# Optimization experiments

Measured on AMD Instinct MI355X. Metric: run time of the kernel, lower is better.

Reference implementation:

```python
import jax, jax.numpy as jnp
import numpy as np

B, NM, NA, D = 16, 4000, 128, 128  # scenes, map nodes/scene, agents/scene, feature dim
DIST_TH = 7.0
BOX = 100.0


def _gn(x, g, b, eps=1e-5):
    # GroupNorm with 1 group over [N, C]: per-row normalization, biased variance, affine.
    mu = jnp.mean(x, axis=-1, keepdims=True)
    var = jnp.mean((x - mu) ** 2, axis=-1, keepdims=True)
    return (x - mu) * jax.lax.rsqrt(var + eps) * g + b


def _forward(feat, turn, control, intersect, agents, map_ctrs, agent_ctrs,
             meta_w, meta_g, meta_b,
             dist_w1, dist_b1, dist_w2, dist_g2, dist_b2,
             query_w, query_g, query_b,
             ctx_w1, ctx_g1, ctx_b1, ctx_w2,
             agt_w, norm_g, norm_b,
             lin_w, lin_g, lin_b,
             hi, wi):
    relu = jax.nn.relu
    # meta fuse: cat(feat, turn, control, intersect) -> Linear(n_map+4 -> n_map) + GN + ReLU
    x = jnp.concatenate([feat, turn, control[:, None], intersect[:, None]], axis=1)
    x = relu(_gn(x @ meta_w.T, meta_g, meta_b))
    for i in range(2):  # two Att layers with distinct weights
        res = x
        d = map_ctrs[hi] - agent_ctrs[wi]                         # [E, 2]
        d = relu(d @ dist_w1[i].T + dist_b1[i])                   # [E, D]
        d = relu(_gn(d @ dist_w2[i].T, dist_g2[i], dist_b2[i]))
        q = relu(_gn(x[hi] @ query_w[i].T, query_g[i], query_b[i]))
        c = jnp.concatenate([d, q, agents[wi]], axis=1)           # [E, 3D]
        c = relu(_gn(c @ ctx_w1[i].T, ctx_g1[i], ctx_b1[i]))
        c = c @ ctx_w2[i].T                                       # [E, D]
        x = x @ agt_w[i].T                                        # [N, D]
        x = x.at[hi].add(c)                                       # index_add_ scatter
        x = relu(_gn(x, norm_g[i], norm_b[i]))
        x = _gn(x @ lin_w[i].T, lin_g[i], lin_b[i])               # Linear act=False
        x = relu(x + res)
    return x


def setup_inputs() -> dict:
    # edge list (hi: map node, wi: agent) built exactly like Att's per-scene dist<=th nonzero
    rng = np.random.default_rng(0)
    mc = rng.uniform(0.0, BOX, (B, NM, 2)).astype(np.float32)
    ac = rng.uniform(0.0, BOX, (B, NA, 2)).astype(np.float32)
    dist = np.sqrt(((mc[:, :, None, :] - ac[:, None, :, :]) ** 2).sum(-1))
    bb, h, w = np.nonzero(dist <= DIST_TH)
    hi = jnp.asarray((bb * NM + h).astype(np.int32))
    wi = jnp.asarray((bb * NA + w).astype(np.int32))

    key = jax.random.key(0)
    ks = jax.random.split(key, 20)
    s = 0.02
    nrm = lambda k, shape: jax.random.normal(k, shape, jnp.float32) * s
    return {
        "feat": jax.random.normal(ks[0], (B * NM, D), jnp.float32),
        "turn": jax.random.normal(ks[1], (B * NM, 2), jnp.float32),
        "control": jax.random.uniform(ks[2], (B * NM,), jnp.float32),
        "intersect": jax.random.uniform(ks[3], (B * NM,), jnp.float32),
        "agents": jax.random.normal(ks[4], (B * NA, D), jnp.float32),
        "map_ctrs": jnp.asarray(mc.reshape(-1, 2)),
        "agent_ctrs": jnp.asarray(ac.reshape(-1, 2)),
        "meta_w": nrm(ks[5], (D, D + 4)),
        "meta_g": jnp.ones((D,), jnp.float32),
        "meta_b": jnp.zeros((D,), jnp.float32),
        "dist_w1": nrm(ks[6], (2, D, 2)),
        "dist_b1": nrm(ks[7], (2, D)),
        "dist_w2": nrm(ks[8], (2, D, D)),
        "dist_g2": jnp.ones((2, D), jnp.float32),
        "dist_b2": jnp.zeros((2, D), jnp.float32),
        "query_w": nrm(ks[9], (2, D, D)),
        "query_g": jnp.ones((2, D), jnp.float32),
        "query_b": jnp.zeros((2, D), jnp.float32),
        "ctx_w1": nrm(ks[10], (2, D, 3 * D)),
        "ctx_g1": jnp.ones((2, D), jnp.float32),
        "ctx_b1": jnp.zeros((2, D), jnp.float32),
        "ctx_w2": nrm(ks[11], (2, D, D)),
        "agt_w": nrm(ks[12], (2, D, D)),
        "norm_g": jnp.ones((2, D), jnp.float32),
        "norm_b": jnp.zeros((2, D), jnp.float32),
        "lin_w": nrm(ks[13], (2, D, D)),
        "lin_g": jnp.ones((2, D), jnp.float32),
        "lin_b": jnp.zeros((2, D), jnp.float32),
        "hi": hi,
        "wi": wi,
    }


def reference(feat, turn, control, intersect, agents, map_ctrs, agent_ctrs,
              meta_w, meta_g, meta_b,
              dist_w1, dist_b1, dist_w2, dist_g2, dist_b2,
              query_w, query_g, query_b,
              ctx_w1, ctx_g1, ctx_b1, ctx_w2,
              agt_w, norm_g, norm_b,
              lin_w, lin_g, lin_b,
              hi, wi):
    return _forward(feat, turn, control, intersect, agents, map_ctrs, agent_ctrs,
                    meta_w, meta_g, meta_b,
                    dist_w1, dist_b1, dist_w2, dist_g2, dist_b2,
                    query_w, query_g, query_b,
                    ctx_w1, ctx_g1, ctx_b1, ctx_w2,
                    agt_w, norm_g, norm_b,
                    lin_w, lin_g, lin_b,
                    hi, wi)
```

## Files before the change

kernel.cpp:

```cpp
#include <hip/hip_runtime.h>


typedef __attribute__((ext_vector_type(8))) short short8v;
typedef __attribute__((ext_vector_type(4))) float f32x4;

#define NXCD 8

__device__ __forceinline__ unsigned short f2b(float f) {
    union { float f; unsigned u; } v; v.f = f;
    return (unsigned short)((v.u + 0x7fffu + ((v.u >> 16) & 1u)) >> 16);
}
__device__ __forceinline__ unsigned pk2(float a, float b) {
    return (unsigned)f2b(a) | ((unsigned)f2b(b) << 16);
}
__device__ __forceinline__ float bflo(unsigned u) { return __uint_as_float(u << 16); }
__device__ __forceinline__ float bfhi(unsigned u) { return __uint_as_float(u & 0xffff0000u); }

union U4S8 { unsigned u[4]; short8v v; };

__device__ __forceinline__ void bar_lds() {
    __builtin_amdgcn_sched_barrier(0);
    asm volatile("s_waitcnt lgkmcnt(0)" ::: "memory");
    __builtin_amdgcn_s_barrier();
    __builtin_amdgcn_sched_barrier(0);
}

template<int NV>
__device__ __forceinline__ void sload(short8v (&v)[NV], const unsigned short* __restrict__ src,
                                      int t) {
#pragma unroll
    for (int i = 0; i < NV; i++) v[i] = *(const short8v*)(src + (size_t)i * 2048 + t * 8);
}
template<int NV>
__device__ __forceinline__ void swrite(unsigned short* dst, const short8v (&v)[NV], int t) {
#pragma unroll
    for (int i = 0; i < NV; i++) *(short8v*)(dst + i * 2048 + t * 8) = v[i];
}

template<int NK>
__device__ __forceinline__ void wgemm_lds(const unsigned short* Wlds,
                                          const short8v* bf, f32x4 (&acc)[8], int l) {
#pragma unroll
    for (int mt = 0; mt < 8; mt++) {
        acc[mt] = (f32x4){0.f, 0.f, 0.f, 0.f};
#pragma unroll
        for (int kk = 0; kk < NK; kk++) {
            const short8v a = *(const short8v*)(Wlds + ((mt * NK + kk) * 64 + l) * 8);
            acc[mt] = __builtin_amdgcn_mfma_f32_16x16x32_bf16(a, bf[kk], acc[mt], 0, 0, 0);
        }
    }
}

__device__ __forceinline__ void gn_apply8(f32x4 (&acc)[8], const float* __restrict__ g,
                                          const float* __restrict__ b, int lg, bool relu) {
    float s = 0.f, s2 = 0.f;
#pragma unroll
    for (int mt = 0; mt < 8; mt++)
#pragma unroll
        for (int q = 0; q < 4; q++) { const float v = acc[mt][q]; s += v; s2 += v * v; }
    s += __shfl_xor(s, 16, 64); s2 += __shfl_xor(s2, 16, 64);
    s += __shfl_xor(s, 32, 64); s2 += __shfl_xor(s2, 32, 64);
    const float mu = s * (1.f / 128.f);
    const float rs = rsqrtf(s2 * (1.f / 128.f) - mu * mu + 1e-5f);
#pragma unroll
    for (int mt = 0; mt < 8; mt++) {
        const f32x4 g4 = *(const f32x4*)(g + mt * 16 + lg * 4);
        const f32x4 b4 = *(const f32x4*)(b + mt * 16 + lg * 4);
#pragma unroll
        for (int q = 0; q < 4; q++) {
            float y = (acc[mt][q] - mu) * rs * g4[q] + b4[q];
            acc[mt][q] = relu ? fmaxf(y, 0.f) : y;
        }
    }
}

__device__ __forceinline__ void pack_p(const f32x4 (&acc)[8], unsigned (&p)[8][2]) {
#pragma unroll
    for (int mt = 0; mt < 8; mt++) {
        p[mt][0] = pk2(acc[mt][0], acc[mt][1]);
        p[mt][1] = pk2(acc[mt][2], acc[mt][3]);
    }
}

__device__ __forceinline__ void lds_put(unsigned short* wbuf, const unsigned (&p)[8][2],
                                        int lg, int col) {
#pragma unroll
    for (int mt = 0; mt < 8; mt++) {
        const unsigned long long v = (unsigned long long)p[mt][0] |
                                     ((unsigned long long)p[mt][1] << 32);
        *(unsigned long long*)((char*)wbuf + ((col * 256 + mt * 32 + lg * 8) ^ ((col & 7) << 4))) = v;
    }
}
__device__ __forceinline__ void lds_wait() {
    asm volatile("s_waitcnt lgkmcnt(0)" ::: "memory");
    __builtin_amdgcn_sched_barrier(0);
}
__device__ __forceinline__ void lds_get(const unsigned short* wbuf, int lg, int col,
                                        short8v* bf) {
#pragma unroll
    for (int kk = 0; kk < 4; kk++)
        bf[kk] = *(const short8v*)((const char*)wbuf +
                 ((col * 256 + kk * 64 + lg * 16) ^ ((col & 7) << 4)));
}
__device__ __forceinline__ void relayout1(unsigned short* wbuf, int lg, int col,
                                          f32x4 (&acc)[8], short8v* bf) {
    unsigned p[8][2];
    pack_p(acc, p); lds_put(wbuf, p, lg, col); lds_wait(); lds_get(wbuf, lg, col, bf);
}

__device__ __forceinline__ void load_bfrag_row(const float* __restrict__ src, int lg,
                                               short8v* bf) {
#pragma unroll
    for (int kk = 0; kk < 4; kk++) {
        const f32x4 a = *(const f32x4*)(src + kk * 32 + lg * 8);
        const f32x4 b = *(const f32x4*)(src + kk * 32 + lg * 8 + 4);
        U4S8 u;
        u.u[0] = pk2(a[0], a[1]); u.u[1] = pk2(a[2], a[3]);
        u.u[2] = pk2(b[0], b[1]); u.u[3] = pk2(b[2], b[3]);
        bf[kk] = u.v;
    }
}
__device__ __forceinline__ void store_rows(float* dst, const f32x4 (&acc)[8], int lg) {
#pragma unroll
    for (int mt = 0; mt < 8; mt++) *(f32x4*)(dst + mt * 16 + lg * 4) = acc[mt];
}
__device__ __forceinline__ void store_rows_bf16(unsigned short* dst, const f32x4 (&acc)[8], int lg) {
#pragma unroll
    for (int mt = 0; mt < 8; mt++) {
        uint2 u; u.x = pk2(acc[mt][0], acc[mt][1]); u.y = pk2(acc[mt][2], acc[mt][3]);
        *(uint2*)(dst + mt * 16 + lg * 4) = u;
    }
}
__device__ __forceinline__ void residual_add_bf16(f32x4 (&acc)[8],
                                                  const unsigned short* __restrict__ rp,
                                                  int lg, bool relu) {
#pragma unroll
    for (int mt = 0; mt < 8; mt++) {
        const uint2 u = *(const uint2*)(rp + mt * 16 + lg * 4);
        acc[mt][0] += bflo(u.x); acc[mt][1] += bfhi(u.x);
        acc[mt][2] += bflo(u.y); acc[mt][3] += bfhi(u.y);
        if (relu) {
#pragma unroll
            for (int q = 0; q < 4; q++) acc[mt][q] = fmaxf(acc[mt][q], 0.f);
        }
    }
}
__device__ __forceinline__ void gather_issue(const unsigned short* __restrict__ Qc,
                                             const unsigned short* __restrict__ Acp,
                                             int h, int w, int lg,
                                             uint2 (&qv)[8], uint2 (&av)[8]) {
    const int hl = (h < 0) ? 0 : h;
    const unsigned short* qp = Qc  + (size_t)hl * 128 + lg * 4;
    const unsigned short* ap = Acp + (size_t)w  * 128 + lg * 4;
#pragma unroll
    for (int mt = 0; mt < 8; mt++) {
        qv[mt] = *(const uint2*)(qp + mt * 16);
        av[mt] = *(const uint2*)(ap + mt * 16);
    }
}
__device__ __forceinline__ void gather_add(f32x4 (&acc)[8], const uint2 (&qv)[8],
                                           const uint2 (&av)[8]) {
#pragma unroll
    for (int mt = 0; mt < 8; mt++) {
        acc[mt][0] += bflo(qv[mt].x) + bflo(av[mt].x);
        acc[mt][1] += bfhi(qv[mt].x) + bfhi(av[mt].x);
        acc[mt][2] += bflo(qv[mt].y) + bflo(av[mt].y);
        acc[mt][3] += bfhi(qv[mt].y) + bfhi(av[mt].y);
    }
}
__device__ __forceinline__ void build_d1(const float* __restrict__ dw1,
                                         const float* __restrict__ db1,
                                         float dx, float dy, int lg, short8v* bf) {
#pragma unroll
    for (int kk = 0; kk < 4; kk++) {
        U4S8 u;
#pragma unroll
        for (int ii = 0; ii < 4; ii++) {
            const int c0 = kk * 32 + lg * 8 + ii * 2;
            const float2 wa = *(const float2*)(dw1 + 2 * c0);
            const float2 wb = *(const float2*)(dw1 + 2 * c0 + 2);
            const float2 bb = *(const float2*)(db1 + c0);
            u.u[ii] = pk2(fmaxf(fmaf(wa.x, dx, fmaf(wa.y, dy, bb.x)), 0.f),
                          fmaxf(fmaf(wb.x, dx, fmaf(wb.y, dy, bb.y)), 0.f));
        }
        bf[kk] = u.v;
    }
}

struct PrepJob { const float* src; int dst; int ld; int kmax; int nk; };
struct PrepJobs { PrepJob j[17]; };

__global__ __launch_bounds__(64) void prep_weights(PrepJobs P, unsigned short* __restrict__ pool) {
    const PrepJob J = P.j[blockIdx.y];
    const int f = blockIdx.x;
    if (f >= 8 * J.nk) return;
    const int l = threadIdx.x;
    const int n = (f / J.nk) * 16 + (l & 15);
    const int kb = (f % J.nk) * 32 + (l >> 4) * 8;
    float v[8];
#pragma unroll
    for (int i = 0; i < 8; i++) {
        const int k = kb + i;
        v[i] = (k < J.kmax) ? J.src[(size_t)n * J.ld + k] : 0.f;
    }
    U4S8 u;
#pragma unroll
    for (int i = 0; i < 4; i++) u.u[i] = pk2(v[2 * i], v[2 * i + 1]);
    *(short8v*)(pool + J.dst + ((size_t)f * 64 + l) * 8) = u.v;
}

__device__ __forceinline__ void agent_path(
    unsigned short* Wlds, int abid, int NA, const float* __restrict__ agents,
    const unsigned short* __restrict__ Wc1a, unsigned short* Ac,
    int t, int wid, int l, int lg, int col)
{
    short8v sv[8];
    sload<8>(sv, Wc1a, t);
    const int r = abid * 64 + wid * 16 + col;
    const int rc = min(r, NA - 1);
    short8v bf[4];
    load_bfrag_row(agents + (size_t)rc * 128, lg, bf);
    swrite<8>(Wlds, sv, t);
    bar_lds();
    f32x4 acc[8];
    wgemm_lds<4>(Wlds, bf, acc, l);
    if (r < NA) store_rows_bf16(Ac + (size_t)r * 128, acc, lg);
}

__global__ __launch_bounds__(256, 2) void meta_node(
    const int N, const int NA, const int gN,
    const float* __restrict__ feat, const float* __restrict__ turn,
    const float* __restrict__ ctrl, const float* __restrict__ inter,
    const float* __restrict__ agents,
    const unsigned short* __restrict__ Wm,
    const float* __restrict__ mg, const float* __restrict__ mb,
    const unsigned short* __restrict__ Wagt, const unsigned short* __restrict__ Wq,
    const float* __restrict__ qg, const float* __restrict__ qb,
    const unsigned short* __restrict__ Wc1q, const unsigned short* __restrict__ Wc1a,
    unsigned short* __restrict__ xA, float* __restrict__ xB,
    unsigned short* __restrict__ Qc, unsigned short* __restrict__ Ac)
{
    __shared__ unsigned short Wlds[20480];
    __shared__ unsigned short wbuf[4][2048];
    const int t = threadIdx.x, wid = t >> 6, l = t & 63, lg = l >> 4, col = l & 15;
    if (blockIdx.x >= gN) {
        agent_path(Wlds, blockIdx.x - gN, NA, agents, Wc1a, Ac, t, wid, l, lg, col);
        return;
    }
    const int r = blockIdx.x * 64 + wid * 16 + col;
    const int rc = min(r, N - 1);

    short8v s10[10];
    sload<10>(s10, Wm, t);
    short8v bf[5];
    load_bfrag_row(feat + (size_t)rc * 128, lg, bf);
    {
        U4S8 u; u.u[0] = 0; u.u[1] = 0; u.u[2] = 0; u.u[3] = 0;
        if (lg == 0) {
            const float2 tv = *(const float2*)(turn + (size_t)rc * 2);
            u.u[0] = pk2(tv.x, tv.y);
            u.u[1] = pk2(ctrl[rc], inter[rc]);
        }
        bf[4] = u.v;
    }
    swrite<10>(Wlds, s10, t);
    bar_lds();

    short8v s8[8];
    sload<8>(s8, Wagt, t);
    f32x4 acc[8];
    wgemm_lds<5>(Wlds, bf, acc, l);
    gn_apply8(acc, mg, mb, lg, true);
    if (r < N) store_rows_bf16(xA + (size_t)r * 128, acc, lg);
    short8v bx[4];
    relayout1(wbuf[wid], lg, col, acc, bx);
    bar_lds();
    swrite<8>(Wlds, s8, t);
    bar_lds();

    sload<8>(s8, Wq, t);
    wgemm_lds<4>(Wlds, bx, acc, l);
    if (r < N) store_rows(xB + (size_t)r * 128, acc, lg);
    bar_lds();
    swrite<8>(Wlds, s8, t);
    bar_lds();

    sload<8>(s8, Wc1q, t);
    wgemm_lds<4>(Wlds, bx, acc, l);
    gn_apply8(acc, qg, qb, lg, true);
    relayout1(wbuf[wid], lg, col, acc, bx);
    bar_lds();
    swrite<8>(Wlds, s8, t);
    bar_lds();

    wgemm_lds<4>(Wlds, bx, acc, l);
    if (r < N) store_rows_bf16(Qc + (size_t)r * 128, acc, lg);
}

__device__ __forceinline__ void post_load_gn(const float* xp,
                                             const float* __restrict__ ng,
                                             const float* __restrict__ nb,
                                             int lg, short8v* bf) {
    float v[4][8];
    float s = 0.f, s2 = 0.f;
#pragma unroll
    for (int kk = 0; kk < 4; kk++) {
        *(f32x4*)(v[kk])     = *(const f32x4*)(xp + kk * 32 + lg * 8);
        *(f32x4*)(v[kk] + 4) = *(const f32x4*)(xp + kk * 32 + lg * 8 + 4);
#pragma unroll
        for (int i = 0; i < 8; i++) { s += v[kk][i]; s2 += v[kk][i] * v[kk][i]; }
    }
    s += __shfl_xor(s, 16, 64); s2 += __shfl_xor(s2, 16, 64);
    s += __shfl_xor(s, 32, 64); s2 += __shfl_xor(s2, 32, 64);
    const float mu = s * (1.f / 128.f);
    const float rs = rsqrtf(s2 * (1.f / 128.f) - mu * mu + 1e-5f);
#pragma unroll
    for (int kk = 0; kk < 4; kk++) {
        float y[8];
#pragma unroll
        for (int i = 0; i < 8; i += 4) {
            const f32x4 g4 = *(const f32x4*)(ng + kk * 32 + lg * 8 + i);
            const f32x4 b4 = *(const f32x4*)(nb + kk * 32 + lg * 8 + i);
#pragma unroll
            for (int q = 0; q < 4; q++)
                y[i + q] = fmaxf((v[kk][i + q] - mu) * rs * g4[q] + b4[q], 0.f);
        }
        U4S8 u;
#pragma unroll
        for (int i = 0; i < 4; i++) u.u[i] = pk2(y[2 * i], y[2 * i + 1]);
        bf[kk] = u.v;
    }
}

__global__ __launch_bounds__(256, 3) void post_node(
    const int N, const int NA, const int gN,
    const float* __restrict__ ng, const float* __restrict__ nb,
    const unsigned short* __restrict__ Wlin,
    const float* __restrict__ lgam, const float* __restrict__ lbet,
    const float* __restrict__ agents, const unsigned short* __restrict__ Wc1a,
    const unsigned short* __restrict__ Wagt, const unsigned short* __restrict__ Wq,
    const float* __restrict__ qg, const float* __restrict__ qb,
    const unsigned short* __restrict__ Wc1q,
    unsigned short* xA, float* xB,
    unsigned short* __restrict__ Qc, unsigned short* __restrict__ Ac)
{
    __shared__ unsigned short Wlds[16384];
    __shared__ unsigned short wbuf[4][2048];
    const int t = threadIdx.x, wid = t >> 6, l = t & 63, lg = l >> 4, col = l & 15;
    if (blockIdx.x >= gN) {
        agent_path(Wlds, blockIdx.x - gN, NA, agents, Wc1a, Ac, t, wid, l, lg, col);
        return;
    }
    const int r = blockIdx.x * 64 + wid * 16 + col;
    const int rc = min(r, N - 1);

    short8v s8[8];
    sload<8>(s8, Wlin, t);
    short8v bf[4];
    post_load_gn(xB + (size_t)rc * 128, ng, nb, lg, bf);
    swrite<8>(Wlds, s8, t);
    bar_lds();

    sload<8>(s8, Wagt, t);
    f32x4 acc[8];
    wgemm_lds<4>(Wlds, bf, acc, l);
    gn_apply8(acc, lgam, lbet, lg, false);
    residual_add_bf16(acc, xA + (size_t)rc * 128, lg, true);
    if (r < N) store_rows_bf16(xA + (size_t)r * 128, acc, lg);
    short8v bx[4];
    relayout1(wbuf[wid], lg, col, acc, bx);
    bar_lds();
    swrite<8>(Wlds, s8, t);
    bar_lds();

    sload<8>(s8, Wq, t);
    wgemm_lds<4>(Wlds, bx, acc, l);
    if (r < N) store_rows(xB + (size_t)r * 128, acc, lg);
    bar_lds();
    swrite<8>(Wlds, s8, t);
    bar_lds();

    sload<8>(s8, Wc1q, t);
    wgemm_lds<4>(Wlds, bx, acc, l);
    gn_apply8(acc, qg, qb, lg, true);
    relayout1(wbuf[wid], lg, col, acc, bx);
    bar_lds();
    swrite<8>(Wlds, s8, t);
    bar_lds();

    wgemm_lds<4>(Wlds, bx, acc, l);
    if (r < N) store_rows_bf16(Qc + (size_t)r * 128, acc, lg);
}

__global__ __launch_bounds__(256, 4) void post_final(
    const int N,
    const float* __restrict__ xB,
    const float* __restrict__ ng, const float* __restrict__ nb,
    const unsigned short* __restrict__ Wlin,
    const float* __restrict__ lgam, const float* __restrict__ lbet,
    const unsigned short* __restrict__ res, float* __restrict__ out)
{
    __shared__ unsigned short Wlds[16384];
    const int t = threadIdx.x, wid = t >> 6, l = t & 63, lg = l >> 4, col = l & 15;
    const int r = blockIdx.x * 64 + wid * 16 + col;
    const int rc = min(r, N - 1);
    short8v s8[8];
    sload<8>(s8, Wlin, t);
    short8v bf[4];
    post_load_gn(xB + (size_t)rc * 128, ng, nb, lg, bf);
    swrite<8>(Wlds, s8, t);
    bar_lds();
    f32x4 acc[8];
    wgemm_lds<4>(Wlds, bf, acc, l);
    gn_apply8(acc, lgam, lbet, lg, false);
    residual_add_bf16(acc, res + (size_t)rc * 128, lg, true);
    if (r < N) store_rows(out + (size_t)r * 128, acc, lg);
}

__global__ __launch_bounds__(256, 3) void edge_mfma(
    const int E, const int nwg,
    const int* __restrict__ hi, const int* __restrict__ wi,
    const float* __restrict__ mc, const float* __restrict__ ac,
    const float* __restrict__ dw1, const float* __restrict__ db1,
    const unsigned short* __restrict__ Wd2, const float* __restrict__ dg2, const float* __restrict__ db2,
    const unsigned short* __restrict__ Wc1d, const float* __restrict__ cg1, const float* __restrict__ cb1,
    const unsigned short* __restrict__ Wc2,
    const unsigned short* __restrict__ Qc, const unsigned short* __restrict__ Acp,
    float* __restrict__ OUT)
{
    __shared__ unsigned short Wlds[16384];
    __shared__ unsigned short wbuf[4][2048];
    __shared__ int s_h[64];
    const int t = threadIdx.x, wid = t >> 6, l = t & 63, lg = l >> 4, col = l & 15;

    int bid;
    {
        const int orig = blockIdx.x;
        const int q = nwg / NXCD, r = nwg % NXCD;
        const int xcd = orig % NXCD, i = orig / NXCD;
        bid = (xcd < r ? xcd * (q + 1) : r * (q + 1) + (xcd - r) * q) + i;
    }
    const int eidx = bid * 64 + wid * 16 + col;

    short8v s8[8];
    sload<8>(s8, Wd2, t);

    int h = -1, w = 0;
    if (eidx < E) { h = hi[eidx]; w = wi[eidx]; }
    if (lg == 0) s_h[wid * 16 + col] = h;
    const int hl = (h < 0) ? 0 : h;
    const float2 mcv = *(const float2*)(mc + 2 * (size_t)hl);
    const float2 acv = *(const float2*)(ac + 2 * (size_t)w);
    const float dx = mcv.x - acv.x, dy = mcv.y - acv.y;

    uint2 qv[8], av[8];
    gather_issue(Qc, Acp, h, w, lg, qv, av);

    short8v bf[4];
    build_d1(dw1, db1, dx, dy, lg, bf);

    swrite<8>(Wlds, s8, t);
    bar_lds();

    sload<8>(s8, Wc1d, t);
    f32x4 acc[8];
    wgemm_lds<4>(Wlds, bf, acc, l);
    gn_apply8(acc, dg2, db2, lg, true);
    relayout1(wbuf[wid], lg, col, acc, bf);
    bar_lds();
    swrite<8>(Wlds, s8, t);
    bar_lds();

    sload<8>(s8, Wc2, t);
    wgemm_lds<4>(Wlds, bf, acc, l);
    gather_add(acc, qv, av);
    gn_apply8(acc, cg1, cb1, lg, true);
    relayout1(wbuf[wid], lg, col, acc, bf);
    bar_lds();
    swrite<8>(Wlds, s8, t);
    bar_lds();

    wgemm_lds<4>(Wlds, bf, acc, l);
    unsigned p[8][2];
    pack_p(acc, p); lds_put(wbuf[wid], p, lg, col); lds_wait();

#pragma unroll
    for (int pass = 0; pass < 2; pass++) {
        const int c = pass * 64 + l;
        float pend = 0.f; int ph = -1;
#pragma unroll
        for (int e = 0; e < 16; e++) {
            const int he = s_h[wid * 16 + e];
            const unsigned short uv = *(const unsigned short*)((const char*)wbuf[wid] +
                                      ((e * 256 + c * 2) ^ ((e & 7) << 4)));
            const float v = __uint_as_float((unsigned)uv << 16);
            if (he == ph) pend += v;
            else {
                if (ph >= 0) atomicAdd(&OUT[(size_t)ph * 128 + c], pend);
                ph = he; pend = v;
            }
        }
        if (ph >= 0) atomicAdd(&OUT[(size_t)ph * 128 + c], pend);
    }
}

extern "C" void kernel_launch(void* const* d_in, const int* in_sizes, int n_in,
                              void* d_out, int out_size, void* d_ws, size_t ws_size,
                              hipStream_t stream)
{
    const float* feat    = (const float*)d_in[0];
    const float* turn    = (const float*)d_in[1];
    const float* ctrl    = (const float*)d_in[2];
    const float* inter   = (const float*)d_in[3];
    const float* agents  = (const float*)d_in[4];
    const float* mc      = (const float*)d_in[5];
    const float* ac      = (const float*)d_in[6];
    const float* meta_w  = (const float*)d_in[7];
    const float* meta_g  = (const float*)d_in[8];
    const float* meta_b  = (const float*)d_in[9];
    const float* dist_w1 = (const float*)d_in[10];
    const float* dist_b1 = (const float*)d_in[11];
    const float* dist_w2 = (const float*)d_in[12];
    const float* dist_g2 = (const float*)d_in[13];
    const float* dist_b2 = (const float*)d_in[14];
    const float* query_w = (const float*)d_in[15];
    const float* query_g = (const float*)d_in[16];
    const float* query_b = (const float*)d_in[17];
    const float* ctx_w1  = (const float*)d_in[18];
    const float* ctx_g1  = (const float*)d_in[19];
    const float* ctx_b1  = (const float*)d_in[20];
    const float* ctx_w2  = (const float*)d_in[21];
    const float* agt_w   = (const float*)d_in[22];
    const float* norm_g  = (const float*)d_in[23];
    const float* norm_b  = (const float*)d_in[24];
    const float* lin_w   = (const float*)d_in[25];
    const float* lin_g   = (const float*)d_in[26];
    const float* lin_b   = (const float*)d_in[27];
    const int*   hi      = (const int*)d_in[28];
    const int*   wi      = (const int*)d_in[29];

    const int E  = in_sizes[28];
    const int N  = in_sizes[0] / 128;
    const int NA = in_sizes[4] / 128;

    unsigned short* xA = (unsigned short*)d_ws;
    float* xB = (float*)(xA + (size_t)N * 128);
    unsigned short* pool = (unsigned short*)(xB + (size_t)N * 128);

    const int FR128  = 8 * 4 * 64 * 8;
    const int FRMETA = 8 * 5 * 64 * 8;
    const int POOL_ELEMS = FRMETA + 16 * FR128;

    unsigned short* Ac = pool + POOL_ELEMS;
    unsigned short* Qc = (unsigned short*)d_out;

    PrepJobs P;
    P.j[0] = { meta_w, 0, 132, 132, 5 };
    for (int i = 0; i < 2; i++) {
        const int b = FRMETA + i * 8 * FR128;
        P.j[1 + i * 8 + 0] = { query_w + (size_t)i * 16384, b + 0 * FR128, 128, 128, 4 };
        P.j[1 + i * 8 + 1] = { agt_w   + (size_t)i * 16384, b + 1 * FR128, 128, 128, 4 };
        P.j[1 + i * 8 + 2] = { dist_w2 + (size_t)i * 16384, b + 2 * FR128, 128, 128, 4 };
        P.j[1 + i * 8 + 3] = { ctx_w1  + (size_t)i * 49152,       b + 3 * FR128, 384, 128, 4 };
        P.j[1 + i * 8 + 4] = { ctx_w1  + (size_t)i * 49152 + 128, b + 4 * FR128, 384, 128, 4 };
        P.j[1 + i * 8 + 5] = { ctx_w2  + (size_t)i * 16384, b + 5 * FR128, 128, 128, 4 };
        P.j[1 + i * 8 + 6] = { lin_w   + (size_t)i * 16384, b + 6 * FR128, 128, 128, 4 };
        P.j[1 + i * 8 + 7] = { ctx_w1  + (size_t)i * 49152 + 256, b + 7 * FR128, 384, 128, 4 };
    }
    prep_weights<<<dim3(40, 17), 64, 0, stream>>>(P, pool);

    const int gN = (N + 63) / 64;
    const int gA = (NA + 63) / 64;
    const int gE = (E + 63) / 64;

    const unsigned short* W0 = pool + FRMETA;
    const unsigned short* W1 = pool + FRMETA + 8 * FR128;

    meta_node<<<gN + gA, 256, 0, stream>>>(
        N, NA, gN, feat, turn, ctrl, inter, agents,
        pool, meta_g, meta_b,
        W0 + 1 * FR128, W0 + 0 * FR128, query_g, query_b,
        W0 + 4 * FR128, W0 + 7 * FR128,
        xA, xB, Qc, Ac);

    edge_mfma<<<gE, 256, 0, stream>>>(
        E, gE, hi, wi, mc, ac,
        dist_w1, dist_b1,
        W0 + 2 * FR128, dist_g2, dist_b2,
        W0 + 3 * FR128, ctx_g1, ctx_b1,
        W0 + 5 * FR128, Qc, Ac, xB);

    post_node<<<gN + gA, 256, 0, stream>>>(
        N, NA, gN,
        norm_g, norm_b, W0 + 6 * FR128, lin_g, lin_b,
        agents, W1 + 7 * FR128,
        W1 + 1 * FR128, W1 + 0 * FR128, query_g + 128, query_b + 128,
        W1 + 4 * FR128,
        xA, xB, Qc, Ac);

    edge_mfma<<<gE, 256, 0, stream>>>(
        E, gE, hi, wi, mc, ac,
        dist_w1 + 256, dist_b1 + 128,
        W1 + 2 * FR128, dist_g2 + 128, dist_b2 + 128,
        W1 + 3 * FR128, ctx_g1 + 128, ctx_b1 + 128,
        W1 + 5 * FR128, Qc, Ac, xB);

    post_final<<<gN, 256, 0, stream>>>(
        N, xB, norm_g + 128, norm_b + 128,
        W1 + 6 * FR128, lin_g + 128, lin_b + 128, xA, (float*)d_out);
}
```

Measured before the change: 202.7 us.

## Process 64 rows per wave to amortize LDS weight staging across four subtiles

Each wave now handles four 16-row subtiles (256 rows per block) in all node, agent, final and edge kernels, so every LDS weight load and barrier is reused across four MFMA passes instead of one. The intent is to cut the per-row cost of staging weight fragments and synchronising, and the grid shrinks by four. The edge kernel also double-buffers the Qc/Ac gathers across subtiles and carries the segmented atomic accumulation across subtiles so runs of equal destination rows merge. Register pressure rises sharply (bf arrays of 4x4 or 4x5), launch bounds drop to 2 blocks per CU, and the smaller grid may underfill the GPU.

After: 259.8 us. 1.28x slower.

```diff
diff --git a/kernel.cpp b/kernel.cpp
--- a/kernel.cpp
+++ b/kernel.cpp
@@ -216,15 +216,20 @@
 {
     short8v sv[8];
     sload<8>(sv, Wc1a, t);
-    const int r = abid * 64 + wid * 16 + col;
-    const int rc = min(r, NA - 1);
-    short8v bf[4];
-    load_bfrag_row(agents + (size_t)rc * 128, lg, bf);
+    const int rbase = abid * 256 + wid * 64;
+    short8v bf[4][4];
+#pragma unroll
+    for (int s = 0; s < 4; s++)
+        load_bfrag_row(agents + (size_t)min(rbase + s * 16 + col, NA - 1) * 128, lg, bf[s]);
     swrite<8>(Wlds, sv, t);
     bar_lds();
     f32x4 acc[8];
-    wgemm_lds<4>(Wlds, bf, acc, l);
-    if (r < NA) store_rows_bf16(Ac + (size_t)r * 128, acc, lg);
+#pragma unroll
+    for (int s = 0; s < 4; s++) {
+        const int r = rbase + s * 16 + col;
+        wgemm_lds<4>(Wlds, bf[s], acc, l);
+        if (r < NA) store_rows_bf16(Ac + (size_t)r * 128, acc, lg);
+    }
 }
 
 __global__ __launch_bounds__(256, 2) void meta_node(
@@ -247,21 +252,22 @@
         agent_path(Wlds, blockIdx.x - gN, NA, agents, Wc1a, Ac, t, wid, l, lg, col);
         return;
     }
-    const int r = blockIdx.x * 64 + wid * 16 + col;
-    const int rc = min(r, N - 1);
+    const int rbase = blockIdx.x * 256 + wid * 64;
 
     short8v s10[10];
     sload<10>(s10, Wm, t);
-    short8v bf[5];
-    load_bfrag_row(feat + (size_t)rc * 128, lg, bf);
-    {
+    short8v bf[4][5];
+#pragma unroll
+    for (int s = 0; s < 4; s++) {
+        const int rc = min(rbase + s * 16 + col, N - 1);
+        load_bfrag_row(feat + (size_t)rc * 128, lg, bf[s]);
         U4S8 u; u.u[0] = 0; u.u[1] = 0; u.u[2] = 0; u.u[3] = 0;
         if (lg == 0) {
             const float2 tv = *(const float2*)(turn + (size_t)rc * 2);
             u.u[0] = pk2(tv.x, tv.y);
             u.u[1] = pk2(ctrl[rc], inter[rc]);
         }
-        bf[4] = u.v;
+        bf[s][4] = u.v;
     }
     swrite<10>(Wlds, s10, t);
     bar_lds();
@@ -269,32 +275,46 @@
     short8v s8[8];
     sload<8>(s8, Wagt, t);
     f32x4 acc[8];
-    wgemm_lds<5>(Wlds, bf, acc, l);
-    gn_apply8(acc, mg, mb, lg, true);
-    if (r < N) store_rows_bf16(xA + (size_t)r * 128, acc, lg);
-    short8v bx[4];
-    relayout1(wbuf[wid], lg, col, acc, bx);
+#pragma unroll
+    for (int s = 0; s < 4; s++) {
+        const int r = rbase + s * 16 + col;
+        wgemm_lds<5>(Wlds, bf[s], acc, l);
+        gn_apply8(acc, mg, mb, lg, true);
+        if (r < N) store_rows_bf16(xA + (size_t)r * 128, acc, lg);
+        relayout1(wbuf[wid], lg, col, acc, bf[s]);
+    }
     bar_lds();
     swrite<8>(Wlds, s8, t);
     bar_lds();
 
     sload<8>(s8, Wq, t);
-    wgemm_lds<4>(Wlds, bx, acc, l);
-    if (r < N) store_rows(xB + (size_t)r * 128, acc, lg);
+#pragma unroll
+    for (int s = 0; s < 4; s++) {
+        const int r = rbase + s * 16 + col;
+        wgemm_lds<4>(Wlds, bf[s], acc, l);
+        if (r < N) store_rows(xB + (size_t)r * 128, acc, lg);
+    }
     bar_lds();
     swrite<8>(Wlds, s8, t);
     bar_lds();
 
     sload<8>(s8, Wc1q, t);
-    wgemm_lds<4>(Wlds, bx, acc, l);
-    gn_apply8(acc, qg, qb, lg, true);
-    relayout1(wbuf[wid], lg, col, acc, bx);
-    bar_lds();
-    swrite<8>(Wlds, s8, t);
-    bar_lds();
-
-    wgemm_lds<4>(Wlds, bx, acc, l);
-    if (r < N) store_rows_bf16(Qc + (size_t)r * 128, acc, lg);
+#pragma unroll
+    for (int s = 0; s < 4; s++) {
+        wgemm_lds<4>(Wlds, bf[s], acc, l);
+        gn_apply8(acc, qg, qb, lg, true);
+        relayout1(wbuf[wid], lg, col, acc, bf[s]);
+    }
+    bar_lds();
+    swrite<8>(Wlds, s8, t);
+    bar_lds();
+
+#pragma unroll
+    for (int s = 0; s < 4; s++) {
+        const int r = rbase + s * 16 + col;
+        wgemm_lds<4>(Wlds, bf[s], acc, l);
+        if (r < N) store_rows_bf16(Qc + (size_t)r * 128, acc, lg);
+    }
 }
 
 __device__ __forceinline__ void post_load_gn(const float* xp,
@@ -332,7 +352,7 @@
     }
 }
 
-__global__ __launch_bounds__(256, 3) void post_node(
+__global__ __launch_bounds__(256, 2) void post_node(
     const int N, const int NA, const int gN,
     const float* __restrict__ ng, const float* __restrict__ nb,
     const unsigned short* __restrict__ Wlin,
@@ -351,48 +371,64 @@
         agent_path(Wlds, blockIdx.x - gN, NA, agents, Wc1a, Ac, t, wid, l, lg, col);
         return;
     }
-    const int r = blockIdx.x * 64 + wid * 16 + col;
-    const int rc = min(r, N - 1);
+    const int rbase = blockIdx.x * 256 + wid * 64;
 
     short8v s8[8];
     sload<8>(s8, Wlin, t);
-    short8v bf[4];
-    post_load_gn(xB + (size_t)rc * 128, ng, nb, lg, bf);
+    short8v bf[4][4];
+#pragma unroll
+    for (int s = 0; s < 4; s++)
+        post_load_gn(xB + (size_t)min(rbase + s * 16 + col, N - 1) * 128, ng, nb, lg, bf[s]);
     swrite<8>(Wlds, s8, t);
     bar_lds();
 
     sload<8>(s8, Wagt, t);
     f32x4 acc[8];
-    wgemm_lds<4>(Wlds, bf, acc, l);
-    gn_apply8(acc, lgam, lbet, lg, false);
-    residual_add_bf16(acc, xA + (size_t)rc * 128, lg, true);
-    if (r < N) store_rows_bf16(xA + (size_t)r * 128, acc, lg);
-    short8v bx[4];
-    relayout1(wbuf[wid], lg, col, acc, bx);
+#pragma unroll
+    for (int s = 0; s < 4; s++) {
+        const int r = rbase + s * 16 + col;
+        const int rc = min(r, N - 1);
+        wgemm_lds<4>(Wlds, bf[s], acc, l);
+        gn_apply8(acc, lgam, lbet, lg, false);
+        residual_add_bf16(acc, xA + (size_t)rc * 128, lg, true);
+        if (r < N) store_rows_bf16(xA + (size_t)r * 128, acc, lg);
+        relayout1(wbuf[wid], lg, col, acc, bf[s]);
+    }
     bar_lds();
     swrite<8>(Wlds, s8, t);
     bar_lds();
 
     sload<8>(s8, Wq, t);
-    wgemm_lds<4>(Wlds, bx, acc, l);
-    if (r < N) store_rows(xB + (size_t)r * 128, acc, lg);
+#pragma unroll
+    for (int s = 0; s < 4; s++) {
+        const int r = rbase + s * 16 + col;
+        wgemm_lds<4>(Wlds, bf[s], acc, l);
+        if (r < N) store_rows(xB + (size_t)r * 128, acc, lg);
+    }
     bar_lds();
     swrite<8>(Wlds, s8, t);
     bar_lds();
 
     sload<8>(s8, Wc1q, t);
-    wgemm_lds<4>(Wlds, bx, acc, l);
-    gn_apply8(acc, qg, qb, lg, true);
-    relayout1(wbuf[wid], lg, col, acc, bx);
-    bar_lds();
-    swrite<8>(Wlds, s8, t);
-    bar_lds();
-
-    wgemm_lds<4>(Wlds, bx, acc, l);
-    if (r < N) store_rows_bf16(Qc + (size_t)r * 128, acc, lg);
-}
-
-__global__ __launch_bounds__(256, 4) void post_final(
+#pragma unroll
+    for (int s = 0; s < 4; s++) {
+        wgemm_lds<4>(Wlds, bf[s], acc, l);
+        gn_apply8(acc, qg, qb, lg, true);
+        relayout1(wbuf[wid], lg, col, acc, bf[s]);
+    }
+    bar_lds();
+    swrite<8>(Wlds, s8, t);
+    bar_lds();
+
+#pragma unroll
+    for (int s = 0; s < 4; s++) {
+        const int r = rbase + s * 16 + col;
+        wgemm_lds<4>(Wlds, bf[s], acc, l);
+        if (r < N) store_rows_bf16(Qc + (size_t)r * 128, acc, lg);
+    }
+}
+
+__global__ __launch_bounds__(256, 2) void post_final(
     const int N,
     const float* __restrict__ xB,
     const float* __restrict__ ng, const float* __restrict__ nb,
@@ -402,22 +438,28 @@
 {
     __shared__ unsigned short Wlds[16384];
     const int t = threadIdx.x, wid = t >> 6, l = t & 63, lg = l >> 4, col = l & 15;
-    const int r = blockIdx.x * 64 + wid * 16 + col;
-    const int rc = min(r, N - 1);
+    const int rbase = blockIdx.x * 256 + wid * 64;
     short8v s8[8];
     sload<8>(s8, Wlin, t);
-    short8v bf[4];
-    post_load_gn(xB + (size_t)rc * 128, ng, nb, lg, bf);
+    short8v bf[4][4];
+#pragma unroll
+    for (int s = 0; s < 4; s++)
+        post_load_gn(xB + (size_t)min(rbase + s * 16 + col, N - 1) * 128, ng, nb, lg, bf[s]);
     swrite<8>(Wlds, s8, t);
     bar_lds();
     f32x4 acc[8];
-    wgemm_lds<4>(Wlds, bf, acc, l);
-    gn_apply8(acc, lgam, lbet, lg, false);
-    residual_add_bf16(acc, res + (size_t)rc * 128, lg, true);
-    if (r < N) store_rows(out + (size_t)r * 128, acc, lg);
-}
-
-__global__ __launch_bounds__(256, 3) void edge_mfma(
+#pragma unroll
+    for (int s = 0; s < 4; s++) {
+        const int r = rbase + s * 16 + col;
+        const int rc = min(r, N - 1);
+        wgemm_lds<4>(Wlds, bf[s], acc, l);
+        gn_apply8(acc, lgam, lbet, lg, false);
+        residual_add_bf16(acc, res + (size_t)rc * 128, lg, true);
+        if (r < N) store_rows(out + (size_t)r * 128, acc, lg);
+    }
+}
+
+__global__ __launch_bounds__(256, 2) void edge_mfma(
     const int E, const int nwg,
     const int* __restrict__ hi, const int* __restrict__ wi,
     const float* __restrict__ mc, const float* __restrict__ ac,
@@ -430,7 +472,7 @@
 {
     __shared__ unsigned short Wlds[16384];
     __shared__ unsigned short wbuf[4][2048];
-    __shared__ int s_h[64];
+    __shared__ int s_h[256];
     const int t = threadIdx.x, wid = t >> 6, l = t & 63, lg = l >> 4, col = l & 15;
 
     int bid;
@@ -440,67 +482,87 @@
         const int xcd = orig % NXCD, i = orig / NXCD;
         bid = (xcd < r ? xcd * (q + 1) : r * (q + 1) + (xcd - r) * q) + i;
     }
-    const int eidx = bid * 64 + wid * 16 + col;
+    const int ebase = bid * 256 + wid * 64;
 
     short8v s8[8];
     sload<8>(s8, Wd2, t);
 
-    int h = -1, w = 0;
-    if (eidx < E) { h = hi[eidx]; w = wi[eidx]; }
-    if (lg == 0) s_h[wid * 16 + col] = h;
-    const int hl = (h < 0) ? 0 : h;
-    const float2 mcv = *(const float2*)(mc + 2 * (size_t)hl);
-    const float2 acv = *(const float2*)(ac + 2 * (size_t)w);
-    const float dx = mcv.x - acv.x, dy = mcv.y - acv.y;
-
-    uint2 qv[8], av[8];
-    gather_issue(Qc, Acp, h, w, lg, qv, av);
-
-    short8v bf[4];
-    build_d1(dw1, db1, dx, dy, lg, bf);
+    int h4[4], w4[4];
+    float dx4[4], dy4[4];
+#pragma unroll
+    for (int s = 0; s < 4; s++) {
+        const int eidx = ebase + s * 16 + col;
+        int h = -1, w = 0;
+        if (eidx < E) { h = hi[eidx]; w = wi[eidx]; }
+        h4[s] = h; w4[s] = w;
+        if (lg == 0) s_h[wid * 64 + s * 16 + col] = h;
+        const int hl = (h < 0) ? 0 : h;
+        const float2 mcv = *(const float2*)(mc + 2 * (size_t)hl);
+        const float2 acv = *(const float2*)(ac + 2 * (size_t)w);
+        dx4[s] = mcv.x - acv.x; dy4[s] = mcv.y - acv.y;
+    }
 
     swrite<8>(Wlds, s8, t);
     bar_lds();
 
     sload<8>(s8, Wc1d, t);
+    short8v bf2[4][4];
     f32x4 acc[8];
-    wgemm_lds<4>(Wlds, bf, acc, l);
-    gn_apply8(acc, dg2, db2, lg, true);
-    relayout1(wbuf[wid], lg, col, acc, bf);
+#pragma unroll
+    for (int s = 0; s < 4; s++) {
+        short8v bft[4];
+        build_d1(dw1, db1, dx4[s], dy4[s], lg, bft);
+        wgemm_lds<4>(Wlds, bft, acc, l);
+        gn_apply8(acc, dg2, db2, lg, true);
+        relayout1(wbuf[wid], lg, col, acc, bf2[s]);
+    }
     bar_lds();
     swrite<8>(Wlds, s8, t);
     bar_lds();
 
     sload<8>(s8, Wc2, t);
-    wgemm_lds<4>(Wlds, bf, acc, l);
-    gather_add(acc, qv, av);
-    gn_apply8(acc, cg1, cb1, lg, true);
-    relayout1(wbuf[wid], lg, col, acc, bf);
-    bar_lds();
-    swrite<8>(Wlds, s8, t);
-    bar_lds();
-
-    wgemm_lds<4>(Wlds, bf, acc, l);
-    unsigned p[8][2];
-    pack_p(acc, p); lds_put(wbuf[wid], p, lg, col); lds_wait();
-
-#pragma unroll
-    for (int pass = 0; pass < 2; pass++) {
-        const int c = pass * 64 + l;
-        float pend = 0.f; int ph = -1;
+    uint2 qv[2][8], av[2][8];
+    gather_issue(Qc, Acp, h4[0], w4[0], lg, qv[0], av[0]);
+#pragma unroll
+    for (int s = 0; s < 4; s++) {
+        if (s < 3) gather_issue(Qc, Acp, h4[s + 1], w4[s + 1], lg, qv[(s + 1) & 1], av[(s + 1) & 1]);
+        wgemm_lds<4>(Wlds, bf2[s], acc, l);
+        gather_add(acc, qv[s & 1], av[s & 1]);
+        gn_apply8(acc, cg1, cb1, lg, true);
+        relayout1(wbuf[wid], lg, col, acc, bf2[s]);
+    }
+    bar_lds();
+    swrite<8>(Wlds, s8, t);
+    bar_lds();
+
+    float p0 = 0.f, p1 = 0.f; int ph = -1;
+#pragma unroll
+    for (int s = 0; s < 4; s++) {
+        wgemm_lds<4>(Wlds, bf2[s], acc, l);
+        unsigned p[8][2];
+        pack_p(acc, p); lds_put(wbuf[wid], p, lg, col); lds_wait();
 #pragma unroll
         for (int e = 0; e < 16; e++) {
-            const int he = s_h[wid * 16 + e];
-            const unsigned short uv = *(const unsigned short*)((const char*)wbuf[wid] +
-                                      ((e * 256 + c * 2) ^ ((e & 7) << 4)));
-            const float v = __uint_as_float((unsigned)uv << 16);
-            if (he == ph) pend += v;
+            const int he = s_h[wid * 64 + s * 16 + e];
+            const unsigned short uA = *(const unsigned short*)((const char*)wbuf[wid] +
+                                      ((e * 256 + l * 2) ^ ((e & 7) << 4)));
+            const unsigned short uB = *(const unsigned short*)((const char*)wbuf[wid] +
+                                      ((e * 256 + (64 + l) * 2) ^ ((e & 7) << 4)));
+            const float vA = __uint_as_float((unsigned)uA << 16);
+            const float vB = __uint_as_float((unsigned)uB << 16);
+            if (he == ph) { p0 += vA; p1 += vB; }
             else {
-                if (ph >= 0) atomicAdd(&OUT[(size_t)ph * 128 + c], pend);
-                ph = he; pend = v;
+                if (ph >= 0) {
+                    atomicAdd(&OUT[(size_t)ph * 128 + l], p0);
+                    atomicAdd(&OUT[(size_t)ph * 128 + 64 + l], p1);
+                }
+                ph = he; p0 = vA; p1 = vB;
             }
         }
-        if (ph >= 0) atomicAdd(&OUT[(size_t)ph * 128 + c], pend);
+    }
+    if (ph >= 0) {
+        atomicAdd(&OUT[(size_t)ph * 128 + l], p0);
+        atomicAdd(&OUT[(size_t)ph * 128 + 64 + l], p1);
     }
 }
 
@@ -569,9 +631,9 @@
     }
     prep_weights<<<dim3(40, 17), 64, 0, stream>>>(P, pool);
 
-    const int gN = (N + 63) / 64;
-    const int gA = (NA + 63) / 64;
-    const int gE = (E + 63) / 64;
+    const int gN = (N + 255) / 256;
+    const int gA = (NA + 255) / 256;
+    const int gE = (E + 255) / 256;
 
     const unsigned short* W0 = pool + FRMETA;
     const unsigned short* W1 = pool + FRMETA + 8 * FR128;
```
